# Kernel optimization log

Measured on AMD Instinct MI355X. Metric: run time of the kernel, lower is better.

The kernel has to match this reference:

```python
import jax, jax.numpy as jnp
import numpy as np

N = 100000
E = 1600000
F_IN = 4
HID = 8
HEADS = 8
NEG_SLOPE = 0.2


def setup_inputs() -> dict:
    key = jax.random.key(0)
    ks = jax.random.split(key, 12)
    x = jax.random.normal(ks[0], (N, F_IN), dtype=jnp.float32)
    edge_index = jax.random.randint(ks[1], (2, E), 0, N, dtype=jnp.int64)
    s = 0.3
    W1 = jax.random.normal(ks[2], (F_IN, HEADS * HID), dtype=jnp.float32) * s
    att_src1 = jax.random.normal(ks[3], (HEADS, HID), dtype=jnp.float32) * s
    att_dst1 = jax.random.normal(ks[4], (HEADS, HID), dtype=jnp.float32) * s
    b1 = jnp.zeros((HEADS * HID,), dtype=jnp.float32)
    W2 = jax.random.normal(ks[5], (HEADS * HID, 1), dtype=jnp.float32) * s
    att_src2 = jax.random.normal(ks[6], (1, 1), dtype=jnp.float32) * s
    att_dst2 = jax.random.normal(ks[7], (1, 1), dtype=jnp.float32) * s
    b2 = jnp.zeros((1,), dtype=jnp.float32)
    return {"x": x, "edge_index": edge_index, "W1": W1, "att_src1": att_src1,
            "att_dst1": att_dst1, "b1": b1, "W2": W2, "att_src2": att_src2,
            "att_dst2": att_dst2, "b2": b2}


def gat_conv(x, src, dst, W, att_s, att_d, b, heads, out_ch, concat):
    n = x.shape[0]
    h = (x @ W).reshape(n, heads, out_ch)              # [N,H,C]
    a_s = jnp.sum(h * att_s, axis=-1)                  # [N,H]
    a_d = jnp.sum(h * att_d, axis=-1)                  # [N,H]
    e = jax.nn.leaky_relu(a_s[src] + a_d[dst], NEG_SLOPE)  # [E,H]
    # segment softmax over edges grouped by destination node
    m = jax.ops.segment_max(e, dst, num_segments=n)
    e = jnp.exp(e - m[dst])
    denom = jax.ops.segment_sum(e, dst, num_segments=n)
    alpha = e / (denom[dst] + 1e-16)                   # [E,H]
    msg = h[src] * alpha[..., None]                    # [E,H,C]
    out = jax.ops.segment_sum(msg, dst, num_segments=n)  # [N,H,C]
    out = out.reshape(n, heads * out_ch) if concat else out.mean(axis=1)
    return out + b


def reference(x, edge_index, W1, att_src1, att_dst1, b1, W2, att_src2, att_dst2, b2):
    n = x.shape[0]
    loops = jnp.arange(n, dtype=edge_index.dtype)
    src = jnp.concatenate([edge_index[0], loops])
    dst = jnp.concatenate([edge_index[1], loops])
    h = gat_conv(x, src, dst, W1, att_src1, att_dst1, b1, HEADS, HID, True)
    h = jax.nn.elu(h)
    out = gat_conv(h, src, dst, W2, att_src2, att_dst2, b2, 1, 1, False)
    return jax.nn.sigmoid(out)
```

## Files before the change

kernel.cpp:

```cpp
#include <hip/hip_runtime.h>

#define NN 100000
#define NE 1600000
#define NBKT 391
#define CAP 8192
#define TILE 16384
#define NTILE ((NE + TILE - 1) / TILE)
#define NEG 0.2f

__global__ __launch_bounds__(512) void kU_prep(
    const float* __restrict__ W1, const float* __restrict__ atts,
    const float* __restrict__ attd, float* __restrict__ us, float* __restrict__ ud,
    int* __restrict__ bcnt)
{
    int t = threadIdx.x;
    if (t < NBKT) bcnt[t] = 0;
    if (t < 64) {
        int half = t >> 5;
        int i = t & 31;
        int h = i >> 2, k = i & 3;
        const float* att = half ? attd : atts;
        float acc = 0.f;
        #pragma unroll
        for (int j = 0; j < 8; j++)
            acc += W1[k * 64 + h * 8 + j] * att[h * 8 + j];
        (half ? ud : us)[h * 4 + k] = acc;
    }
}

__global__ __launch_bounds__(1024) void kP1_tile(
    const int* __restrict__ ei, int* __restrict__ bcnt, unsigned* __restrict__ bpack)
{
    __shared__ unsigned sarr[TILE];
    __shared__ int lh[512], lsc[512], lgb[512];
    int t = threadIdx.x;
    int e0 = blockIdx.x * TILE;
    int n = NE - e0; if (n > TILE) n = TILE;

    if (t < 512) lh[t] = 0;
    __syncthreads();
    for (int i = t; i < n; i += 1024) {
        int d = ei[NE + e0 + i];
        atomicAdd(&lh[d >> 8], 1);
    }
    __syncthreads();
    if (t < 512) lsc[t] = lh[t];
    __syncthreads();
    #pragma unroll
    for (int o = 1; o < 512; o <<= 1) {
        int u = 0;
        if (t < 512 && t >= o) u = lsc[t - o];
        __syncthreads();
        if (t < 512) lsc[t] += u;
        __syncthreads();
    }
    if (t < NBKT && lh[t] > 0) lgb[t] = atomicAdd(&bcnt[t], lh[t]);
    __syncthreads();
    if (t < 512) lh[t] = lsc[t] - lh[t];
    __syncthreads();
    for (int i = t; i < n; i += 1024) {
        int s = ei[e0 + i], d = ei[NE + e0 + i];
        int b = d >> 8;
        int pos = atomicAdd(&lh[b], 1);
        sarr[pos] = ((unsigned)s << 8) | (unsigned)(d & 255);
    }
    __syncthreads();
    int wave = t >> 6, lane = t & 63;
    for (int b = wave; b < NBKT; b += 16) {
        int start = (b == 0) ? 0 : lsc[b - 1];
        int cntb = lsc[b] - start;
        if (cntb == 0) continue;
        int gb = lgb[b];
        unsigned* dstp = &bpack[(size_t)b * CAP];
        for (int j = lane; j < cntb; j += 64) {
            int gpos = gb + j;
            if (gpos < CAP) dstp[gpos] = sarr[start + j];
        }
    }
}

__global__ __launch_bounds__(512) void kS_scan(
    const int* __restrict__ bcnt, int* __restrict__ bktoff, int* __restrict__ row)
{
    __shared__ int s[512];
    int t = threadIdx.x;
    int v = (t < NBKT) ? bcnt[t] : 0;
    s[t] = v;
    __syncthreads();
    #pragma unroll
    for (int o = 1; o < 512; o <<= 1) {
        int u = (t >= o) ? s[t - o] : 0;
        __syncthreads();
        s[t] += u;
        __syncthreads();
    }
    if (t < NBKT) bktoff[t] = s[t] - v;
    if (t == 0) row[NN] = NE;
}

__global__ __launch_bounds__(1024) void kP2_build(
    const int* __restrict__ bcnt, const int* __restrict__ bktoff,
    const unsigned* __restrict__ bpack, int* __restrict__ row, int* __restrict__ esrc)
{
    __shared__ int lh[256], lsc[256], lcur[256];
    __shared__ int sarr[CAP];
    int b = blockIdx.x;
    int t = threadIdx.x;
    int cnt = bcnt[b];
    if (cnt > CAP) cnt = CAP;
    const unsigned* bp = &bpack[(size_t)b * CAP];
    if (t < 256) lh[t] = 0;
    __syncthreads();
    for (int i = t; i < cnt; i += 1024)
        atomicAdd(&lh[bp[i] & 255u], 1);
    __syncthreads();
    if (t < 256) lsc[t] = lh[t];
    __syncthreads();
    #pragma unroll
    for (int o = 1; o < 256; o <<= 1) {
        int u = 0;
        if (t < 256 && t >= o) u = lsc[t - o];
        __syncthreads();
        if (t < 256) lsc[t] += u;
        __syncthreads();
    }
    int base = bktoff[b];
    if (t < 256) {
        int ex = lsc[t] - lh[t];
        lcur[t] = ex;
        int node = b * 256 + t;
        if (node < NN) row[node] = base + ex;
    }
    __syncthreads();
    for (int i = t; i < cnt; i += 1024) {
        unsigned u = bp[i];
        int pos = atomicAdd(&lcur[u & 255u], 1);
        sarr[pos] = (int)(u >> 8);
    }
    __syncthreads();
    for (int i = t; i < cnt; i += 1024)
        esrc[base + i] = sarr[i];
}

__global__ __launch_bounds__(256) void kE_l1agg(
    const int* __restrict__ row, const int* __restrict__ esrc,
    const float* __restrict__ x, const float* __restrict__ us,
    const float* __restrict__ ud, const float* __restrict__ W1,
    const float* __restrict__ b1, const float* __restrict__ W2,
    float* __restrict__ h2)
{
    int t = threadIdx.x;
    int grp = t >> 4;
    int sub = t & 15;
    int dst = blockIdx.x * 16 + grp;
    if (dst >= NN) return;
    int slot = sub >> 3;
    int h    = sub & 7;

    int start = row[dst], end = row[dst + 1];
    int m = end - start;

    float4 u  = *reinterpret_cast<const float4*>(&us[h * 4]);
    float4 vd = *reinterpret_cast<const float4*>(&ud[h * 4]);
    float4 xd = *reinterpret_cast<const float4*>(&x[(size_t)dst * 4]);
    float adj = xd.x * vd.x + xd.y * vd.y + xd.z * vd.z + xd.w * vd.w;

    float xa0 = 0.f, xa1 = 0.f, xa2 = 0.f, xa3 = 0.f, den = 0.f;
    for (int j = slot; j <= m; j += 2) {
        int s = (j < m) ? esrc[start + j] : dst;
        float4 xs = *reinterpret_cast<const float4*>(&x[(size_t)s * 4]);
        float a = fmaf(xs.x, u.x, fmaf(xs.y, u.y, fmaf(xs.z, u.z, fmaf(xs.w, u.w, adj))));
        a = fmaxf(a, NEG * a);
        float p = __expf(a);
        den += p;
        xa0 = fmaf(p, xs.x, xa0);
        xa1 = fmaf(p, xs.y, xa1);
        xa2 = fmaf(p, xs.z, xa2);
        xa3 = fmaf(p, xs.w, xa3);
    }
    xa0 += __shfl_xor(xa0, 8, 16);
    xa1 += __shfl_xor(xa1, 8, 16);
    xa2 += __shfl_xor(xa2, 8, 16);
    xa3 += __shfl_xor(xa3, 8, 16);
    den += __shfl_xor(den, 8, 16);

    int c0 = h * 8 + slot * 4;
    float4 w0 = *reinterpret_cast<const float4*>(&W1[c0]);
    float4 w1 = *reinterpret_cast<const float4*>(&W1[64 + c0]);
    float4 w2 = *reinterpret_cast<const float4*>(&W1[128 + c0]);
    float4 w3 = *reinterpret_cast<const float4*>(&W1[192 + c0]);
    float4 bb = *reinterpret_cast<const float4*>(&b1[c0]);
    float4 ww = *reinterpret_cast<const float4*>(&W2[c0]);
    float inv = 1.f / (den + 1e-16f);

    float acc;
    {
        float v = (xa0 * w0.x + xa1 * w1.x + xa2 * w2.x + xa3 * w3.x) * inv + bb.x;
        v = v > 0.f ? v : (__expf(v) - 1.f);
        acc = v * ww.x;
    }
    {
        float v = (xa0 * w0.y + xa1 * w1.y + xa2 * w2.y + xa3 * w3.y) * inv + bb.y;
        v = v > 0.f ? v : (__expf(v) - 1.f);
        acc += v * ww.y;
    }
    {
        float v = (xa0 * w0.z + xa1 * w1.z + xa2 * w2.z + xa3 * w3.z) * inv + bb.z;
        v = v > 0.f ? v : (__expf(v) - 1.f);
        acc += v * ww.z;
    }
    {
        float v = (xa0 * w0.w + xa1 * w1.w + xa2 * w2.w + xa3 * w3.w) * inv + bb.w;
        v = v > 0.f ? v : (__expf(v) - 1.f);
        acc += v * ww.w;
    }
    #pragma unroll
    for (int o = 1; o < 16; o <<= 1) acc += __shfl_xor(acc, o, 16);
    if (sub == 0) h2[dst] = acc;
}

__global__ __launch_bounds__(256) void kF_l2agg(
    const int* __restrict__ row, const int* __restrict__ esrc,
    const float* __restrict__ h2, const float* __restrict__ as2,
    const float* __restrict__ ad2, const float* __restrict__ b2,
    float* __restrict__ out)
{
    int grp = threadIdx.x >> 4;
    int sub = threadIdx.x & 15;
    int dst = blockIdx.x * 16 + grp;
    if (dst >= NN) return;
    int start = row[dst], end = row[dst + 1];
    float a_s = as2[0], a_d = ad2[0];
    float hdv = h2[dst];
    float hd = hdv * a_d;

    float den = 0.f, num = 0.f;
    if (sub == 0) {
        float v = hdv * a_s + hd;
        v = fmaxf(v, NEG * v);
        float p = __expf(v);
        den = p;
        num = p * hdv;
    }
    for (int i = start + sub; i < end; i += 16) {
        float hs = h2[esrc[i]];
        float v = hs * a_s + hd;
        v = fmaxf(v, NEG * v);
        float p = __expf(v);
        den += p;
        num += p * hs;
    }
    #pragma unroll
    for (int o = 8; o; o >>= 1) {
        den += __shfl_xor(den, o, 16);
        num += __shfl_xor(num, o, 16);
    }
    if (sub == 0) {
        float v = num / (den + 1e-16f) + b2[0];
        out[dst] = 1.f / (1.f + __expf(-v));
    }
}

extern "C" void kernel_launch(void* const* d_in, const int* in_sizes, int n_in,
                              void* d_out, int out_size, void* d_ws, size_t ws_size,
                              hipStream_t stream) {
    const float* x     = (const float*)d_in[0];
    const int*   ei    = (const int*)d_in[1];
    const float* W1    = (const float*)d_in[2];
    const float* atts1 = (const float*)d_in[3];
    const float* attd1 = (const float*)d_in[4];
    const float* b1    = (const float*)d_in[5];
    const float* W2    = (const float*)d_in[6];
    const float* atts2 = (const float*)d_in[7];
    const float* attd2 = (const float*)d_in[8];
    const float* b2    = (const float*)d_in[9];
    float* out = (float*)d_out;

    float* w = (float*)d_ws;
    float* us = w;
    float* ud = w + 32;
    float* h2 = w + 64;
    int* ibase  = (int*)(w + 64 + (size_t)NN);
    int* bcnt   = ibase;
    int* bktoff = ibase + 512;
    int* row    = ibase + 1024;
    int* esrc   = ibase + 1024 + NN + 64;
    unsigned* bpack = (unsigned*)(ibase + 1024 + NN + 64 + NE);

    dim3 gG((NN + 15) / 16);

    hipLaunchKernelGGL(kU_prep, dim3(1), dim3(512), 0, stream, W1, atts1, attd1, us, ud, bcnt);
    hipLaunchKernelGGL(kP1_tile, dim3(NTILE), dim3(1024), 0, stream, ei, bcnt, bpack);
    hipLaunchKernelGGL(kS_scan, dim3(1), dim3(512), 0, stream, bcnt, bktoff, row);
    hipLaunchKernelGGL(kP2_build, dim3(NBKT), dim3(1024), 0, stream, bcnt, bktoff, bpack, row, esrc);
    hipLaunchKernelGGL(kE_l1agg, gG, dim3(256), 0, stream, row, esrc, x, us, ud, W1, b1, W2, h2);
    hipLaunchKernelGGL(kF_l2agg, gG, dim3(256), 0, stream, row, esrc, h2, atts2, attd2, b2, out);
}
```

Before: 78.87 us.

## Use 8 lanes per destination node and unroll edge loops by two

Both aggregation kernels now assign 8 threads per destination node instead of 16, so each block covers 32 nodes. In layer 1 each thread owns one head and walks all of that node's edges, with the self-loop handled up front and the loop unrolled by two. In layer 2 the edge loop is unrolled by two and the shuffle reduction is shortened to 8 lanes. The binning tile size is also cut from 16384 to 4096, which launches more tiles. The aim is fewer shuffles and more loads in flight, at the cost of less parallelism per node and more serial work per thread on high-degree nodes.

```diff
diff --git a/kernel.cpp b/kernel.cpp
--- a/kernel.cpp
+++ b/kernel.cpp
@@ -4,7 +4,7 @@
 #define NE 1600000
 #define NBKT 391
 #define CAP 8192
-#define TILE 16384
+#define TILE 4096
 #define NTILE ((NE + TILE - 1) / TILE)
 #define NEG 0.2f
 
@@ -150,12 +150,10 @@
     float* __restrict__ h2)
 {
     int t = threadIdx.x;
-    int grp = t >> 4;
-    int sub = t & 15;
-    int dst = blockIdx.x * 16 + grp;
+    int grp = t >> 3;
+    int h   = t & 7;
+    int dst = blockIdx.x * 32 + grp;
     if (dst >= NN) return;
-    int slot = sub >> 3;
-    int h    = sub & 7;
 
     int start = row[dst], end = row[dst + 1];
     int m = end - start;
@@ -165,58 +163,82 @@
     float4 xd = *reinterpret_cast<const float4*>(&x[(size_t)dst * 4]);
     float adj = xd.x * vd.x + xd.y * vd.y + xd.z * vd.z + xd.w * vd.w;
 
-    float xa0 = 0.f, xa1 = 0.f, xa2 = 0.f, xa3 = 0.f, den = 0.f;
-    for (int j = slot; j <= m; j += 2) {
-        int s = (j < m) ? esrc[start + j] : dst;
-        float4 xs = *reinterpret_cast<const float4*>(&x[(size_t)s * 4]);
-        float a = fmaf(xs.x, u.x, fmaf(xs.y, u.y, fmaf(xs.z, u.z, fmaf(xs.w, u.w, adj))));
-        a = fmaxf(a, NEG * a);
-        float p = __expf(a);
-        den += p;
-        xa0 = fmaf(p, xs.x, xa0);
-        xa1 = fmaf(p, xs.y, xa1);
-        xa2 = fmaf(p, xs.z, xa2);
-        xa3 = fmaf(p, xs.w, xa3);
-    }
-    xa0 += __shfl_xor(xa0, 8, 16);
-    xa1 += __shfl_xor(xa1, 8, 16);
-    xa2 += __shfl_xor(xa2, 8, 16);
-    xa3 += __shfl_xor(xa3, 8, 16);
-    den += __shfl_xor(den, 8, 16);
-
-    int c0 = h * 8 + slot * 4;
-    float4 w0 = *reinterpret_cast<const float4*>(&W1[c0]);
-    float4 w1 = *reinterpret_cast<const float4*>(&W1[64 + c0]);
-    float4 w2 = *reinterpret_cast<const float4*>(&W1[128 + c0]);
-    float4 w3 = *reinterpret_cast<const float4*>(&W1[192 + c0]);
-    float4 bb = *reinterpret_cast<const float4*>(&b1[c0]);
-    float4 ww = *reinterpret_cast<const float4*>(&W2[c0]);
+    float a0 = fmaf(xd.x, u.x, fmaf(xd.y, u.y, fmaf(xd.z, u.z, fmaf(xd.w, u.w, adj))));
+    a0 = fmaxf(a0, NEG * a0);
+    float p0 = __expf(a0);
+    float den = p0;
+    float xa0 = p0 * xd.x, xa1 = p0 * xd.y, xa2 = p0 * xd.z, xa3 = p0 * xd.w;
+
+    int j = 0;
+    for (; j + 2 <= m; j += 2) {
+        int s0 = esrc[start + j];
+        int s1 = esrc[start + j + 1];
+        float4 q0 = *reinterpret_cast<const float4*>(&x[(size_t)s0 * 4]);
+        float4 q1 = *reinterpret_cast<const float4*>(&x[(size_t)s1 * 4]);
+        float b0 = fmaf(q0.x, u.x, fmaf(q0.y, u.y, fmaf(q0.z, u.z, fmaf(q0.w, u.w, adj))));
+        float c1 = fmaf(q1.x, u.x, fmaf(q1.y, u.y, fmaf(q1.z, u.z, fmaf(q1.w, u.w, adj))));
+        b0 = fmaxf(b0, NEG * b0);
+        c1 = fmaxf(c1, NEG * c1);
+        float pb = __expf(b0);
+        float pc = __expf(c1);
+        den += pb + pc;
+        xa0 = fmaf(pb, q0.x, fmaf(pc, q1.x, xa0));
+        xa1 = fmaf(pb, q0.y, fmaf(pc, q1.y, xa1));
+        xa2 = fmaf(pb, q0.z, fmaf(pc, q1.z, xa2));
+        xa3 = fmaf(pb, q0.w, fmaf(pc, q1.w, xa3));
+    }
+    if (j < m) {
+        int s0 = esrc[start + j];
+        float4 q0 = *reinterpret_cast<const float4*>(&x[(size_t)s0 * 4]);
+        float b0 = fmaf(q0.x, u.x, fmaf(q0.y, u.y, fmaf(q0.z, u.z, fmaf(q0.w, u.w, adj))));
+        b0 = fmaxf(b0, NEG * b0);
+        float pb = __expf(b0);
+        den += pb;
+        xa0 = fmaf(pb, q0.x, xa0);
+        xa1 = fmaf(pb, q0.y, xa1);
+        xa2 = fmaf(pb, q0.z, xa2);
+        xa3 = fmaf(pb, q0.w, xa3);
+    }
+
+    int c0 = h * 8;
+    float4 w0l = *reinterpret_cast<const float4*>(&W1[c0]);
+    float4 w0h = *reinterpret_cast<const float4*>(&W1[c0 + 4]);
+    float4 w1l = *reinterpret_cast<const float4*>(&W1[64 + c0]);
+    float4 w1h = *reinterpret_cast<const float4*>(&W1[64 + c0 + 4]);
+    float4 w2l = *reinterpret_cast<const float4*>(&W1[128 + c0]);
+    float4 w2h = *reinterpret_cast<const float4*>(&W1[128 + c0 + 4]);
+    float4 w3l = *reinterpret_cast<const float4*>(&W1[192 + c0]);
+    float4 w3h = *reinterpret_cast<const float4*>(&W1[192 + c0 + 4]);
+    float4 bbl = *reinterpret_cast<const float4*>(&b1[c0]);
+    float4 bbh = *reinterpret_cast<const float4*>(&b1[c0 + 4]);
+    float4 wwl = *reinterpret_cast<const float4*>(&W2[c0]);
+    float4 wwh = *reinterpret_cast<const float4*>(&W2[c0 + 4]);
     float inv = 1.f / (den + 1e-16f);
 
-    float acc;
+    float acc = 0.f;
     {
-        float v = (xa0 * w0.x + xa1 * w1.x + xa2 * w2.x + xa3 * w3.x) * inv + bb.x;
-        v = v > 0.f ? v : (__expf(v) - 1.f);
-        acc = v * ww.x;
-    }
-    {
-        float v = (xa0 * w0.y + xa1 * w1.y + xa2 * w2.y + xa3 * w3.y) * inv + bb.y;
-        v = v > 0.f ? v : (__expf(v) - 1.f);
-        acc += v * ww.y;
-    }
-    {
-        float v = (xa0 * w0.z + xa1 * w1.z + xa2 * w2.z + xa3 * w3.z) * inv + bb.z;
-        v = v > 0.f ? v : (__expf(v) - 1.f);
-        acc += v * ww.z;
-    }
-    {
-        float v = (xa0 * w0.w + xa1 * w1.w + xa2 * w2.w + xa3 * w3.w) * inv + bb.w;
-        v = v > 0.f ? v : (__expf(v) - 1.f);
-        acc += v * ww.w;
-    }
-    #pragma unroll
-    for (int o = 1; o < 16; o <<= 1) acc += __shfl_xor(acc, o, 16);
-    if (sub == 0) h2[dst] = acc;
+        float v;
+        v = (xa0*w0l.x + xa1*w1l.x + xa2*w2l.x + xa3*w3l.x)*inv + bbl.x;
+        v = v > 0.f ? v : (__expf(v) - 1.f);  acc += v * wwl.x;
+        v = (xa0*w0l.y + xa1*w1l.y + xa2*w2l.y + xa3*w3l.y)*inv + bbl.y;
+        v = v > 0.f ? v : (__expf(v) - 1.f);  acc += v * wwl.y;
+        v = (xa0*w0l.z + xa1*w1l.z + xa2*w2l.z + xa3*w3l.z)*inv + bbl.z;
+        v = v > 0.f ? v : (__expf(v) - 1.f);  acc += v * wwl.z;
+        v = (xa0*w0l.w + xa1*w1l.w + xa2*w2l.w + xa3*w3l.w)*inv + bbl.w;
+        v = v > 0.f ? v : (__expf(v) - 1.f);  acc += v * wwl.w;
+        v = (xa0*w0h.x + xa1*w1h.x + xa2*w2h.x + xa3*w3h.x)*inv + bbh.x;
+        v = v > 0.f ? v : (__expf(v) - 1.f);  acc += v * wwh.x;
+        v = (xa0*w0h.y + xa1*w1h.y + xa2*w2h.y + xa3*w3h.y)*inv + bbh.y;
+        v = v > 0.f ? v : (__expf(v) - 1.f);  acc += v * wwh.y;
+        v = (xa0*w0h.z + xa1*w1h.z + xa2*w2h.z + xa3*w3h.z)*inv + bbh.z;
+        v = v > 0.f ? v : (__expf(v) - 1.f);  acc += v * wwh.z;
+        v = (xa0*w0h.w + xa1*w1h.w + xa2*w2h.w + xa3*w3h.w)*inv + bbh.w;
+        v = v > 0.f ? v : (__expf(v) - 1.f);  acc += v * wwh.w;
+    }
+    acc += __shfl_xor(acc, 1, 8);
+    acc += __shfl_xor(acc, 2, 8);
+    acc += __shfl_xor(acc, 4, 8);
+    if (h == 0) h2[dst] = acc;
 }
 
 __global__ __launch_bounds__(256) void kF_l2agg(
@@ -225,9 +247,10 @@
     const float* __restrict__ ad2, const float* __restrict__ b2,
     float* __restrict__ out)
 {
-    int grp = threadIdx.x >> 4;
-    int sub = threadIdx.x & 15;
-    int dst = blockIdx.x * 16 + grp;
+    int t = threadIdx.x;
+    int grp = t >> 3;
+    int sub = t & 7;
+    int dst = blockIdx.x * 32 + grp;
     if (dst >= NN) return;
     int start = row[dst], end = row[dst + 1];
     float a_s = as2[0], a_d = ad2[0];
@@ -242,19 +265,33 @@
         den = p;
         num = p * hdv;
     }
-    for (int i = start + sub; i < end; i += 16) {
+    int i = start + sub;
+    for (; i + 8 < end; i += 16) {
+        float hs0 = h2[esrc[i]];
+        float hs1 = h2[esrc[i + 8]];
+        float v0 = hs0 * a_s + hd;
+        float v1 = hs1 * a_s + hd;
+        v0 = fmaxf(v0, NEG * v0);
+        v1 = fmaxf(v1, NEG * v1);
+        float p0 = __expf(v0);
+        float p1 = __expf(v1);
+        den += p0 + p1;
+        num = fmaf(p0, hs0, fmaf(p1, hs1, num));
+    }
+    if (i < end) {
         float hs = h2[esrc[i]];
         float v = hs * a_s + hd;
         v = fmaxf(v, NEG * v);
         float p = __expf(v);
         den += p;
-        num += p * hs;
-    }
-    #pragma unroll
-    for (int o = 8; o; o >>= 1) {
-        den += __shfl_xor(den, o, 16);
-        num += __shfl_xor(num, o, 16);
-    }
+        num = fmaf(p, hs, num);
+    }
+    den += __shfl_xor(den, 1, 8);
+    num += __shfl_xor(num, 1, 8);
+    den += __shfl_xor(den, 2, 8);
+    num += __shfl_xor(num, 2, 8);
+    den += __shfl_xor(den, 4, 8);
+    num += __shfl_xor(num, 4, 8);
     if (sub == 0) {
         float v = num / (den + 1e-16f) + b2[0];
         out[dst] = 1.f / (1.f + __expf(-v));
@@ -287,7 +324,7 @@
     int* esrc   = ibase + 1024 + NN + 64;
     unsigned* bpack = (unsigned*)(ibase + 1024 + NN + 64 + NE);
 
-    dim3 gG((NN + 15) / 16);
+    dim3 gG((NN + 31) / 32);
 
     hipLaunchKernelGGL(kU_prep, dim3(1), dim3(512), 0, stream, W1, atts1, attd1, us, ud, bcnt);
     hipLaunchKernelGGL(kP1_tile, dim3(NTILE), dim3(1024), 0, stream, ei, bcnt, bpack);
```

New measurement: 75.58 us. 1.04x faster.
